# Kernel optimization log

Hardware: AMD Instinct MI355X
Metric: run time of the kernel (lower is better)

Reference implementation:

```python
import jax, jax.numpy as jnp
import numpy as np

PF_DIM = 1024
F_DIM = 1024
LOW = 128
MID = 32  # low_dim // 4
BATCH = 8192


def setup_inputs() -> dict:
    key = jax.random.key(0)
    ks = jax.random.split(key, 10)
    s = lambda fan_in: 1.0 / np.sqrt(fan_in)
    return {
        "f": jax.random.normal(ks[0], (BATCH, F_DIM), jnp.float32),
        "pf": jax.random.normal(ks[1], (BATCH, PF_DIM), jnp.float32),
        # nn.Linear weights are (out, in)
        "proj_f_w": jax.random.uniform(ks[2], (LOW, F_DIM), jnp.float32, -s(F_DIM), s(F_DIM)),
        "proj_f_b": jax.random.uniform(ks[3], (LOW,), jnp.float32, -s(F_DIM), s(F_DIM)),
        "proj_pf_w": jax.random.uniform(ks[4], (LOW, PF_DIM), jnp.float32, -s(PF_DIM), s(PF_DIM)),
        "proj_pf_b": jax.random.uniform(ks[5], (LOW,), jnp.float32, -s(PF_DIM), s(PF_DIM)),
        "proj_f2_w": jax.random.uniform(ks[6], (F_DIM, LOW), jnp.float32, -s(LOW), s(LOW)),
        "proj_f2_b": jax.random.uniform(ks[7], (F_DIM,), jnp.float32, -s(LOW), s(LOW)),
        "pg_w": jax.random.uniform(ks[8], (2 * LOW * MID, LOW), jnp.float32, -s(LOW), s(LOW)),
        "pg_b": jax.random.uniform(ks[9], (2 * LOW * MID,), jnp.float32, -s(LOW), s(LOW)),
    }


def reference(f, pf, proj_f_w, proj_f_b, proj_pf_w, proj_pf_b,
              proj_f2_w, proj_f2_b, pg_w, pg_b):
    b = pf.shape[0]
    # project both inputs to low_dim
    f_low = f @ proj_f_w.T + proj_f_b              # (b, LOW)
    pf_low = pf @ proj_pf_w.T + proj_pf_b          # (b, LOW)
    # per-sample generated weights
    params = pf_low @ pg_w.T + pg_b                # (b, 2*LOW*MID)
    dim = LOW * MID
    p1 = params[:, :dim].reshape(b, LOW, MID)      # (b, LOW, MID)
    p2 = params[:, dim:].reshape(b, MID, LOW)      # (b, MID, LOW)
    # batched tiny MLP: (b,1,LOW)@(b,LOW,MID) -> relu -> @(b,MID,LOW)
    h = jax.nn.relu(jnp.einsum('bl,blm->bm', f_low, p1))
    g = jnp.einsum('bm,bml->bl', h, p2)            # (b, LOW)
    out = g @ proj_f2_w.T + proj_f2_b + f + pf     # (b, F_DIM)
    return out
```

## Files before the change

kernel.cpp:

```cpp
#include <hip/hip_runtime.h>
#include <stdint.h>


typedef __attribute__((ext_vector_type(8))) short bf16x8;
typedef __attribute__((ext_vector_type(4))) float f32x4;

#define MFMA(a, b, c) __builtin_amdgcn_mfma_f32_16x16x32_bf16((a), (b), (c), 0, 0, 0)

__device__ __forceinline__ ushort f2bf(float x) {
    union { float f; uint32_t u; } v; v.f = x;
    return (ushort)((v.u + 0x7FFFu + ((v.u >> 16) & 1u)) >> 16);
}
__device__ __forceinline__ ushort4 f2bf4(float4 v) {
    ushort4 o; o.x = f2bf(v.x); o.y = f2bf(v.y); o.z = f2bf(v.z); o.w = f2bf(v.w); return o;
}
__device__ __forceinline__ float bf2f(ushort u) {
    union { uint32_t i; float f; } v; v.i = ((uint32_t)u) << 16; return v.f;
}

__global__ __launch_bounds__(256) void k0_convert(
    const float* __restrict__ pgw, const float* __restrict__ wf,
    const float* __restrict__ wpf, const float* __restrict__ w2,
    ushort* __restrict__ pg_img, ushort* __restrict__ w_img, ushort* __restrict__ w2_img)
{
    int cid = blockIdx.x * 256 + threadIdx.x;
    const float* src; ushort* dst;
    if (cid < 131072) {
        int lane = cid & 63, ks = (cid >> 6) & 3, T = cid >> 8;
        int j = T * 16 + (lane & 15), k = ks * 32 + (lane >> 4) * 8;
        src = pgw + (size_t)j * 128 + k;
        dst = pg_img + (size_t)cid * 8;
    } else if (cid < 163840) {
        int c = cid - 131072;
        int lane = c & 63, ks = (c >> 6) & 31, lt = (c >> 11) & 7, mat = c >> 14;
        int l = lt * 16 + (lane & 15), k = ks * 32 + (lane >> 4) * 8;
        src = (mat ? wpf : wf) + (size_t)l * 1024 + k;
        dst = w_img + (size_t)c * 8;
    } else {
        int c = cid - 163840;
        int lane = c & 63, ks = (c >> 6) & 3, nt = c >> 8;
        int n = nt * 16 + (lane & 15), k = ks * 32 + (lane >> 4) * 8;
        src = w2 + (size_t)n * 128 + k;
        dst = w2_img + (size_t)c * 8;
    }
    float4 a = ((const float4*)src)[0], b = ((const float4*)src)[1];
    ((ushort4*)dst)[0] = f2bf4(a);
    ((ushort4*)dst)[1] = f2bf4(b);
}

__global__ __launch_bounds__(512, 2) void mega(
    const float* __restrict__ f, const float* __restrict__ pf,
    const ushort* __restrict__ w_img, const float* __restrict__ bfb,
    const float* __restrict__ bpfb, const ushort* __restrict__ pg_img,
    const float* __restrict__ pgb, const ushort* __restrict__ w2_img,
    const float* __restrict__ b2, float* __restrict__ out)
{
    __shared__ __align__(16) char smem[62464];
    ushort* As    = (ushort*)smem;
    ushort* Tr    = (ushort*)smem;
    float*  hred  = (float*)smem;
    float*  hl    = (float*)(smem + 32768);
    float*  gred  = (float*)smem;
    float*  Ls    = (float*)smem;
    ushort* flowT = (ushort*)(smem + 36864);
    ushort* pfrag = (ushort*)(smem + 46080);
    ushort* gfrag = (ushort*)(smem + 54272);

    const int tid = threadIdx.x;
    const int lane = tid & 63, wid = tid >> 6;
    const int q = lane >> 4, r15 = lane & 15;
    const int b0 = blockIdx.x * 32;

    {
        float4 vbuf[8];
#pragma unroll
        for (int rr = 0; rr < 8; rr++) {
            int row = rr * 4 + (tid >> 7);
            vbuf[rr] = *(const float4*)(f + (size_t)(b0 + row) * 1024 + (tid & 127) * 4);
        }
        f32x4 c[2];
        float bias_v = 0.f;
#pragma unroll
        for (int s = 0; s < 4; s++) {
            const int mat = s >> 1, kh = s & 1;
            if (kh == 0) {
                c[0] = (f32x4){0.f, 0.f, 0.f, 0.f};
                c[1] = (f32x4){0.f, 0.f, 0.f, 0.f};
                bias_v = (mat ? bpfb : bfb)[wid * 16 + r15];
            }
            __syncthreads();
#pragma unroll
            for (int rr = 0; rr < 8; rr++) {
                int row = rr * 4 + (tid >> 7);
                *(ushort4*)(As + row * 520 + (tid & 127) * 4) = f2bf4(vbuf[rr]);
            }
            __syncthreads();
            if (s < 3) {
                const int sn = s + 1, matn = sn >> 1, khn = sn & 1;
                const float* srcn = matn ? pf : f;
#pragma unroll
                for (int rr = 0; rr < 8; rr++) {
                    int row = rr * 4 + (tid >> 7);
                    vbuf[rr] = *(const float4*)(srcn + (size_t)(b0 + row) * 1024 + khn * 512 + (tid & 127) * 4);
                }
            }
            const ushort* wb = w_img + (size_t)mat * 131072 + ((size_t)wid * 32 + kh * 16) * 512;
            bf16x8 wfr[4];
#pragma unroll
            for (int p = 0; p < 4; p++) wfr[p] = *(const bf16x8*)(wb + (size_t)p * 512 + lane * 8);
#pragma unroll
            for (int ks = 0; ks < 16; ks++) {
                const int cur = ks & 3;
                bf16x8 a0 = *(const bf16x8*)(As + (size_t)r15 * 520 + ks * 32 + q * 8);
                bf16x8 a1 = *(const bf16x8*)(As + (size_t)(16 + r15) * 520 + ks * 32 + q * 8);
                c[0] = MFMA(a0, wfr[cur], c[0]);
                c[1] = MFMA(a1, wfr[cur], c[1]);
                if (ks + 4 < 16)
                    wfr[cur] = *(const bf16x8*)(wb + (size_t)(ks + 4) * 512 + lane * 8);
            }
            if (s == 1) {
                int l = wid * 16 + r15;
#pragma unroll
                for (int mt = 0; mt < 2; mt++)
#pragma unroll
                    for (int r = 0; r < 4; r++)
                        flowT[l * 36 + mt * 16 + q * 4 + r] = f2bf(c[mt][r] + bias_v);
            }
            if (s == 3) {
                __syncthreads();
                int l = wid * 16 + r15;
#pragma unroll
                for (int mt = 0; mt < 2; mt++)
#pragma unroll
                    for (int r = 0; r < 4; r++)
                        Tr[(mt * 16 + q * 4 + r) * 136 + l] = f2bf(c[mt][r] + bias_v);
                __syncthreads();
                int bt = wid >> 2, ks2 = wid & 3;
                int k0 = ks2 * 32 + (lane >> 4) * 8;
                uint4 tv = *(const uint4*)(Tr + (size_t)(bt * 16 + (lane & 15)) * 136 + k0);
                *(uint4*)(pfrag + (size_t)wid * 512 + lane * 8) = tv;
            }
        }
    }
    __syncthreads();

    bf16x8 bfr[2][4];
#pragma unroll
    for (int ct = 0; ct < 2; ct++)
#pragma unroll
        for (int ks = 0; ks < 4; ks++)
            bfr[ct][ks] = *(const bf16x8*)(pfrag + (size_t)(ct * 4 + ks) * 512 + lane * 8);

    f32x4 hacc[2][2];
    hacc[0][0] = hacc[0][1] = hacc[1][0] = hacc[1][1] = (f32x4){0.f, 0.f, 0.f, 0.f};

    {
        bf16x8 af[4][4];
        f32x4 bvr[4];
#pragma unroll
        for (int t = 0; t < 4; t++) {
            const int tl = wid * 4 + t;
            const ushort* ap = pg_img + (size_t)tl * 2048;
#pragma unroll
            for (int ks = 0; ks < 4; ks++)
                af[t][ks] = *(const bf16x8*)(ap + ks * 512 + lane * 8);
            bvr[t] = *(const f32x4*)(pgb + (size_t)tl * 16 + q * 4);
        }
#pragma unroll
        for (int jg = 0; jg < 8; jg++) {
#pragma unroll
            for (int i = 0; i < 4; i++) {
                const int t = jg * 4 + i, cur = t & 3;
                const int tl = wid * 4 + i;
                const int mh = i & 1;
                const int l_loc = tl >> 1;
                f32x4 bv = bvr[cur];
#pragma unroll
                for (int ct = 0; ct < 2; ct++) {
                    f32x4 cc = (f32x4){0.f, 0.f, 0.f, 0.f};
#pragma unroll
                    for (int ks = 0; ks < 4; ks++) cc = MFMA(af[cur][ks], bfr[ct][ks], cc);
                    float s = bf2f(flowT[(jg * 16 + l_loc) * 36 + ct * 16 + r15]);
#pragma unroll
                    for (int r = 0; r < 4; r++) hacc[mh][ct][r] += s * (cc[r] + bv[r]);
                }
                if (t + 4 < 32) {
                    const int tn = t + 4, jgn = tn >> 2, in = tn & 3;
                    const int tln = jgn * 32 + wid * 4 + in;
                    const ushort* ap = pg_img + (size_t)tln * 2048;
#pragma unroll
                    for (int ks = 0; ks < 4; ks++)
                        af[cur][ks] = *(const bf16x8*)(ap + ks * 512 + lane * 8);
                    bvr[cur] = *(const f32x4*)(pgb + (size_t)tln * 16 + q * 4);
                }
            }
        }
    }
#pragma unroll
    for (int mh = 0; mh < 2; mh++)
#pragma unroll
        for (int ct = 0; ct < 2; ct++)
#pragma unroll
            for (int r = 0; r < 4; r++)
                hred[wid * 1024 + (mh * 16 + q * 4 + r) * 32 + ct * 16 + r15] = hacc[mh][ct][r];
    __syncthreads();
    {
        int m = tid >> 4, bc = (tid & 15) * 2;
        float s0 = 0.f, s1 = 0.f;
#pragma unroll
        for (int w = 0; w < 8; w++) {
            s0 += hred[w * 1024 + m * 32 + bc];
            s1 += hred[w * 1024 + m * 32 + bc + 1];
        }
        hl[m * 32 + bc]     = fmaxf(s0, 0.f);
        hl[m * 32 + bc + 1] = fmaxf(s1, 0.f);
    }
    __syncthreads();

    {
        bf16x8 afc[4][4];
        f32x4 bvc[4];
#pragma unroll
        for (int t = 0; t < 4; t++) {
            const int m = wid + 8 * (t >> 1), lt = t & 1;
            const ushort* ap = pg_img + (size_t)(256 + m * 8 + lt) * 2048;
#pragma unroll
            for (int ks = 0; ks < 4; ks++)
                afc[t][ks] = *(const bf16x8*)(ap + ks * 512 + lane * 8);
            bvc[t] = *(const f32x4*)(pgb + 4096 + (size_t)m * 128 + lt * 16 + q * 4);
        }
#pragma unroll
        for (int lg = 0; lg < 4; lg++) {
            f32x4 gacc[2][2];
            gacc[0][0] = gacc[0][1] = gacc[1][0] = gacc[1][1] = (f32x4){0.f, 0.f, 0.f, 0.f};
#pragma unroll
            for (int ti = 0; ti < 8; ti++) {
                const int t = lg * 8 + ti, cur = t & 3;
                const int m = wid + 8 * (ti >> 1), lt = ti & 1;
                f32x4 bv = bvc[cur];
#pragma unroll
                for (int ct = 0; ct < 2; ct++) {
                    f32x4 cc = (f32x4){0.f, 0.f, 0.f, 0.f};
#pragma unroll
                    for (int ks = 0; ks < 4; ks++) cc = MFMA(afc[cur][ks], bfr[ct][ks], cc);
                    float s = hl[m * 32 + ct * 16 + r15];
#pragma unroll
                    for (int r = 0; r < 4; r++) gacc[lt][ct][r] += s * (cc[r] + bv[r]);
                }
                if (t + 4 < 32) {
                    const int tn = t + 4, lgn = tn >> 3, tin = tn & 7;
                    const int mn = wid + 8 * (tin >> 1), ltn = tin & 1;
                    const ushort* ap = pg_img + (size_t)(256 + mn * 8 + lgn * 2 + ltn) * 2048;
#pragma unroll
                    for (int ks = 0; ks < 4; ks++)
                        afc[cur][ks] = *(const bf16x8*)(ap + ks * 512 + lane * 8);
                    bvc[cur] = *(const f32x4*)(pgb + 4096 + (size_t)mn * 128 + lgn * 32 + ltn * 16 + q * 4);
                }
            }
#pragma unroll
            for (int lt = 0; lt < 2; lt++)
#pragma unroll
                for (int ct = 0; ct < 2; ct++)
#pragma unroll
                    for (int r = 0; r < 4; r++)
                        gred[wid * 1024 + (lt * 16 + q * 4 + r) * 32 + ct * 16 + r15] = gacc[lt][ct][r];
            __syncthreads();
            if (tid < 128) {
                int bt = tid >> 6, ln = tid & 63;
                int b_loc = bt * 16 + (ln & 15);
                int l0 = (ln >> 4) * 8;
                ushort tmp[8];
#pragma unroll
                for (int e = 0; e < 8; e++) {
                    const float* gp = gred + (size_t)(l0 + e) * 32 + b_loc;
                    float s = 0.f;
#pragma unroll
                    for (int w = 0; w < 8; w++) s += gp[w * 1024];
                    tmp[e] = f2bf(s);
                }
                ushort4 lo = {tmp[0], tmp[1], tmp[2], tmp[3]};
                ushort4 hi = {tmp[4], tmp[5], tmp[6], tmp[7]};
                ushort* dst = gfrag + (size_t)(bt * 4 + lg) * 512 + ln * 8;
                ((ushort4*)dst)[0] = lo;
                ((ushort4*)dst)[1] = hi;
            }
            __syncthreads();
        }
    }

    {
        bf16x8 afg[2][4];
#pragma unroll
        for (int mtl = 0; mtl < 2; mtl++)
#pragma unroll
            for (int ks = 0; ks < 4; ks++)
                afg[mtl][ks] = *(const bf16x8*)(gfrag + (size_t)(mtl * 4 + ks) * 512 + lane * 8);

        bf16x8 w2r[2][2][4];
#pragma unroll
        for (int nt = 0; nt < 2; nt++)
#pragma unroll
            for (int ks = 0; ks < 4; ks++)
                w2r[0][nt][ks] = *(const bf16x8*)(w2_img + (size_t)((wid * 2 + nt) * 4 + ks) * 512 + lane * 8);

#pragma unroll
        for (int nb = 0; nb < 4; nb++) {
            const int cur = nb & 1;
            const int n0 = nb * 256;
            float4 fa[4], pa[4];
#pragma unroll
            for (int rr = 0; rr < 4; rr++) {
                const int b = b0 + wid * 4 + rr;
                const size_t gbase = (size_t)b * 1024 + n0 + lane * 4;
                fa[rr] = *(const float4*)(f + gbase);
                pa[rr] = *(const float4*)(pf + gbase);
            }
            float bias_v2[2];
#pragma unroll
            for (int nt = 0; nt < 2; nt++) bias_v2[nt] = b2[nb * 256 + wid * 32 + nt * 16 + r15];
#pragma unroll
            for (int nt = 0; nt < 2; nt++) {
#pragma unroll
                for (int mtl = 0; mtl < 2; mtl++) {
                    f32x4 cc = (f32x4){0.f, 0.f, 0.f, 0.f};
#pragma unroll
                    for (int ks = 0; ks < 4; ks++) cc = MFMA(afg[mtl][ks], w2r[cur][nt][ks], cc);
                    const int nloc = wid * 32 + nt * 16 + r15;
                    const int chunk = nloc >> 5, within = nloc & 31;
#pragma unroll
                    for (int r = 0; r < 4; r++)
                        Ls[(size_t)(mtl * 16 + q * 4 + r) * 288 + chunk * 36 + within] = cc[r] + bias_v2[nt];
                }
            }
            if (nb < 3) {
#pragma unroll
                for (int nt = 0; nt < 2; nt++)
#pragma unroll
                    for (int ks = 0; ks < 4; ks++)
                        w2r[cur ^ 1][nt][ks] = *(const bf16x8*)(w2_img + (size_t)(((nb + 1) * 16 + wid * 2 + nt) * 4 + ks) * 512 + lane * 8);
            }
            __syncthreads();
            {
                const float* ls = Ls + (size_t)(wid * 4) * 288 + (lane >> 3) * 36 + (lane & 7) * 4;
#pragma unroll
                for (int rr = 0; rr < 4; rr++) {
                    const int b = b0 + wid * 4 + rr;
                    const size_t gbase = (size_t)b * 1024 + n0 + lane * 4;
                    float4 lv = *(const float4*)(ls + rr * 288);
                    float4 o;
                    o.x = lv.x + fa[rr].x + pa[rr].x; o.y = lv.y + fa[rr].y + pa[rr].y;
                    o.z = lv.z + fa[rr].z + pa[rr].z; o.w = lv.w + fa[rr].w + pa[rr].w;
                    *(float4*)(out + gbase) = o;
                }
            }
            __syncthreads();
        }
    }
}

extern "C" void kernel_launch(void* const* d_in, const int* in_sizes, int n_in,
                              void* d_out, int out_size, void* d_ws, size_t ws_size,
                              hipStream_t stream)
{
    const float* f    = (const float*)d_in[0];
    const float* pf   = (const float*)d_in[1];
    const float* wf   = (const float*)d_in[2];
    const float* bfb  = (const float*)d_in[3];
    const float* wpf  = (const float*)d_in[4];
    const float* bpfb = (const float*)d_in[5];
    const float* w2   = (const float*)d_in[6];
    const float* b2   = (const float*)d_in[7];
    const float* pgw  = (const float*)d_in[8];
    const float* pgb  = (const float*)d_in[9];

    char* ws = (char*)d_ws;
    ushort* pg_img = (ushort*)(ws + 0);
    ushort* w_img  = (ushort*)(ws + 2097152);
    ushort* w2_img = (ushort*)(ws + 2621440);
    float*  out    = (float*)d_out;

    k0_convert<<<dim3(704), dim3(256), 0, stream>>>(pgw, wf, wpf, w2, pg_img, w_img, w2_img);
    mega<<<dim3(256), dim3(512), 0, stream>>>(f, pf, w_img, bfb, bpfb,
                                              pg_img, pgb, w2_img, b2, out);
}
```

Before: 176.5 us.

## Repartition hypernet weight-gen work across waves to shrink cross-wave reductions

Reassigns the two per-sample weight-generation phases so each wave owns a fixed output slice (mh and l-quarter in phase one, one l-tile in phase two) and accumulates over the contracted index itself. Phase one's cross-wave reduction now sums 4 partials instead of 8. Phase two's per-group LDS reductions and their barriers are removed. Both reduction buffers gain a padded stride of 33 to avoid bank conflicts. W2 register double-buffering is dropped in favour of in-loop loads, which lowers register pressure but exposes load latency.

```diff
diff --git a/kernel.cpp b/kernel.cpp
--- a/kernel.cpp
+++ b/kernel.cpp
@@ -59,8 +59,8 @@
     ushort* As    = (ushort*)smem;
     ushort* Tr    = (ushort*)smem;
     float*  hred  = (float*)smem;
-    float*  hl    = (float*)(smem + 32768);
-    float*  gred  = (float*)smem;
+    float*  hl    = (float*)(smem + 16896);
+    float*  gLDS  = (float*)smem;
     float*  Ls    = (float*)smem;
     ushort* flowT = (ushort*)(smem + 36864);
     ushort* pfrag = (ushort*)(smem + 46080);
@@ -151,66 +151,58 @@
         for (int ks = 0; ks < 4; ks++)
             bfr[ct][ks] = *(const bf16x8*)(pfrag + (size_t)(ct * 4 + ks) * 512 + lane * 8);
 
-    f32x4 hacc[2][2];
-    hacc[0][0] = hacc[0][1] = hacc[1][0] = hacc[1][1] = (f32x4){0.f, 0.f, 0.f, 0.f};
-
-    {
+    {
+        const int mh = wid & 1, lq = wid >> 1;
+        f32x4 hacc[2];
+        hacc[0] = (f32x4){0.f, 0.f, 0.f, 0.f};
+        hacc[1] = (f32x4){0.f, 0.f, 0.f, 0.f};
+
         bf16x8 af[4][4];
-        f32x4 bvr[4];
 #pragma unroll
         for (int t = 0; t < 4; t++) {
-            const int tl = wid * 4 + t;
-            const ushort* ap = pg_img + (size_t)tl * 2048;
+            const int T = (lq * 32 + t) * 2 + mh;
+            const ushort* ap = pg_img + (size_t)T * 2048;
 #pragma unroll
             for (int ks = 0; ks < 4; ks++)
                 af[t][ks] = *(const bf16x8*)(ap + ks * 512 + lane * 8);
-            bvr[t] = *(const f32x4*)(pgb + (size_t)tl * 16 + q * 4);
-        }
-#pragma unroll
-        for (int jg = 0; jg < 8; jg++) {
-#pragma unroll
-            for (int i = 0; i < 4; i++) {
-                const int t = jg * 4 + i, cur = t & 3;
-                const int tl = wid * 4 + i;
-                const int mh = i & 1;
-                const int l_loc = tl >> 1;
-                f32x4 bv = bvr[cur];
-#pragma unroll
-                for (int ct = 0; ct < 2; ct++) {
-                    f32x4 cc = (f32x4){0.f, 0.f, 0.f, 0.f};
-#pragma unroll
-                    for (int ks = 0; ks < 4; ks++) cc = MFMA(af[cur][ks], bfr[ct][ks], cc);
-                    float s = bf2f(flowT[(jg * 16 + l_loc) * 36 + ct * 16 + r15]);
-#pragma unroll
-                    for (int r = 0; r < 4; r++) hacc[mh][ct][r] += s * (cc[r] + bv[r]);
-                }
-                if (t + 4 < 32) {
-                    const int tn = t + 4, jgn = tn >> 2, in = tn & 3;
-                    const int tln = jgn * 32 + wid * 4 + in;
-                    const ushort* ap = pg_img + (size_t)tln * 2048;
-#pragma unroll
-                    for (int ks = 0; ks < 4; ks++)
-                        af[cur][ks] = *(const bf16x8*)(ap + ks * 512 + lane * 8);
-                    bvr[cur] = *(const f32x4*)(pgb + (size_t)tln * 16 + q * 4);
-                }
-            }
-        }
-    }
-#pragma unroll
-    for (int mh = 0; mh < 2; mh++)
+        }
+#pragma unroll
+        for (int t = 0; t < 32; t++) {
+            const int cur = t & 3;
+            const int l = lq * 32 + t;
+            const int T = l * 2 + mh;
+            f32x4 bv = *(const f32x4*)(pgb + (size_t)T * 16 + q * 4);
+#pragma unroll
+            for (int ct = 0; ct < 2; ct++) {
+                f32x4 cc = (f32x4){0.f, 0.f, 0.f, 0.f};
+#pragma unroll
+                for (int ks = 0; ks < 4; ks++) cc = MFMA(af[cur][ks], bfr[ct][ks], cc);
+                float s = bf2f(flowT[l * 36 + ct * 16 + r15]);
+#pragma unroll
+                for (int r = 0; r < 4; r++) hacc[ct][r] += s * (cc[r] + bv[r]);
+            }
+            if (t + 4 < 32) {
+                const int Tn = (l + 4) * 2 + mh;
+                const ushort* ap = pg_img + (size_t)Tn * 2048;
+#pragma unroll
+                for (int ks = 0; ks < 4; ks++)
+                    af[cur][ks] = *(const bf16x8*)(ap + ks * 512 + lane * 8);
+            }
+        }
 #pragma unroll
         for (int ct = 0; ct < 2; ct++)
 #pragma unroll
             for (int r = 0; r < 4; r++)
-                hred[wid * 1024 + (mh * 16 + q * 4 + r) * 32 + ct * 16 + r15] = hacc[mh][ct][r];
+                hred[lq * 1056 + (mh * 16 + q * 4 + r) * 33 + ct * 16 + r15] = hacc[ct][r];
+    }
     __syncthreads();
     {
         int m = tid >> 4, bc = (tid & 15) * 2;
         float s0 = 0.f, s1 = 0.f;
 #pragma unroll
-        for (int w = 0; w < 8; w++) {
-            s0 += hred[w * 1024 + m * 32 + bc];
-            s1 += hred[w * 1024 + m * 32 + bc + 1];
+        for (int w = 0; w < 4; w++) {
+            s0 += hred[w * 1056 + m * 33 + bc];
+            s1 += hred[w * 1056 + m * 33 + bc + 1];
         }
         hl[m * 32 + bc]     = fmaxf(s0, 0.f);
         hl[m * 32 + bc + 1] = fmaxf(s1, 0.f);
@@ -218,75 +210,61 @@
     __syncthreads();
 
     {
+        f32x4 gacc[2];
+        gacc[0] = (f32x4){0.f, 0.f, 0.f, 0.f};
+        gacc[1] = (f32x4){0.f, 0.f, 0.f, 0.f};
+
         bf16x8 afc[4][4];
-        f32x4 bvc[4];
 #pragma unroll
         for (int t = 0; t < 4; t++) {
-            const int m = wid + 8 * (t >> 1), lt = t & 1;
-            const ushort* ap = pg_img + (size_t)(256 + m * 8 + lt) * 2048;
+            const ushort* ap = pg_img + (size_t)(256 + t * 8 + wid) * 2048;
 #pragma unroll
             for (int ks = 0; ks < 4; ks++)
                 afc[t][ks] = *(const bf16x8*)(ap + ks * 512 + lane * 8);
-            bvc[t] = *(const f32x4*)(pgb + 4096 + (size_t)m * 128 + lt * 16 + q * 4);
-        }
-#pragma unroll
-        for (int lg = 0; lg < 4; lg++) {
-            f32x4 gacc[2][2];
-            gacc[0][0] = gacc[0][1] = gacc[1][0] = gacc[1][1] = (f32x4){0.f, 0.f, 0.f, 0.f};
-#pragma unroll
-            for (int ti = 0; ti < 8; ti++) {
-                const int t = lg * 8 + ti, cur = t & 3;
-                const int m = wid + 8 * (ti >> 1), lt = ti & 1;
-                f32x4 bv = bvc[cur];
-#pragma unroll
-                for (int ct = 0; ct < 2; ct++) {
-                    f32x4 cc = (f32x4){0.f, 0.f, 0.f, 0.f};
-#pragma unroll
-                    for (int ks = 0; ks < 4; ks++) cc = MFMA(afc[cur][ks], bfr[ct][ks], cc);
-                    float s = hl[m * 32 + ct * 16 + r15];
-#pragma unroll
-                    for (int r = 0; r < 4; r++) gacc[lt][ct][r] += s * (cc[r] + bv[r]);
-                }
-                if (t + 4 < 32) {
-                    const int tn = t + 4, lgn = tn >> 3, tin = tn & 7;
-                    const int mn = wid + 8 * (tin >> 1), ltn = tin & 1;
-                    const ushort* ap = pg_img + (size_t)(256 + mn * 8 + lgn * 2 + ltn) * 2048;
-#pragma unroll
-                    for (int ks = 0; ks < 4; ks++)
-                        afc[cur][ks] = *(const bf16x8*)(ap + ks * 512 + lane * 8);
-                    bvc[cur] = *(const f32x4*)(pgb + 4096 + (size_t)mn * 128 + lgn * 32 + ltn * 16 + q * 4);
-                }
-            }
-#pragma unroll
-            for (int lt = 0; lt < 2; lt++)
-#pragma unroll
-                for (int ct = 0; ct < 2; ct++)
-#pragma unroll
-                    for (int r = 0; r < 4; r++)
-                        gred[wid * 1024 + (lt * 16 + q * 4 + r) * 32 + ct * 16 + r15] = gacc[lt][ct][r];
-            __syncthreads();
-            if (tid < 128) {
-                int bt = tid >> 6, ln = tid & 63;
-                int b_loc = bt * 16 + (ln & 15);
-                int l0 = (ln >> 4) * 8;
-                ushort tmp[8];
-#pragma unroll
-                for (int e = 0; e < 8; e++) {
-                    const float* gp = gred + (size_t)(l0 + e) * 32 + b_loc;
-                    float s = 0.f;
-#pragma unroll
-                    for (int w = 0; w < 8; w++) s += gp[w * 1024];
-                    tmp[e] = f2bf(s);
-                }
-                ushort4 lo = {tmp[0], tmp[1], tmp[2], tmp[3]};
-                ushort4 hi = {tmp[4], tmp[5], tmp[6], tmp[7]};
-                ushort* dst = gfrag + (size_t)(bt * 4 + lg) * 512 + ln * 8;
-                ((ushort4*)dst)[0] = lo;
-                ((ushort4*)dst)[1] = hi;
-            }
-            __syncthreads();
-        }
-    }
+        }
+#pragma unroll
+        for (int m = 0; m < 32; m++) {
+            const int cur = m & 3;
+            f32x4 bv = *(const f32x4*)(pgb + 4096 + (size_t)m * 128 + wid * 16 + q * 4);
+#pragma unroll
+            for (int ct = 0; ct < 2; ct++) {
+                f32x4 cc = (f32x4){0.f, 0.f, 0.f, 0.f};
+#pragma unroll
+                for (int ks = 0; ks < 4; ks++) cc = MFMA(afc[cur][ks], bfr[ct][ks], cc);
+                float s = hl[m * 32 + ct * 16 + r15];
+#pragma unroll
+                for (int r = 0; r < 4; r++) gacc[ct][r] += s * (cc[r] + bv[r]);
+            }
+            if (m + 4 < 32) {
+                const int mn = m + 4;
+                const ushort* ap = pg_img + (size_t)(256 + mn * 8 + wid) * 2048;
+#pragma unroll
+                for (int ks = 0; ks < 4; ks++)
+                    afc[cur][ks] = *(const bf16x8*)(ap + ks * 512 + lane * 8);
+            }
+        }
+#pragma unroll
+        for (int ct = 0; ct < 2; ct++)
+#pragma unroll
+            for (int r = 0; r < 4; r++)
+                gLDS[(size_t)(wid * 16 + q * 4 + r) * 33 + ct * 16 + r15] = gacc[ct][r];
+    }
+    __syncthreads();
+    {
+        const int bt = wid >> 2, ksl = wid & 3;
+        const int bloc = bt * 16 + (lane & 15);
+        const int l0 = ksl * 32 + (lane >> 4) * 8;
+        ushort tmp[8];
+#pragma unroll
+        for (int e = 0; e < 8; e++)
+            tmp[e] = f2bf(gLDS[(size_t)(l0 + e) * 33 + bloc]);
+        ushort4 lo = {tmp[0], tmp[1], tmp[2], tmp[3]};
+        ushort4 hi = {tmp[4], tmp[5], tmp[6], tmp[7]};
+        ushort* dst = gfrag + (size_t)wid * 512 + lane * 8;
+        ((ushort4*)dst)[0] = lo;
+        ((ushort4*)dst)[1] = hi;
+    }
+    __syncthreads();
 
     {
         bf16x8 afg[2][4];
@@ -296,16 +274,8 @@
             for (int ks = 0; ks < 4; ks++)
                 afg[mtl][ks] = *(const bf16x8*)(gfrag + (size_t)(mtl * 4 + ks) * 512 + lane * 8);
 
-        bf16x8 w2r[2][2][4];
-#pragma unroll
-        for (int nt = 0; nt < 2; nt++)
-#pragma unroll
-            for (int ks = 0; ks < 4; ks++)
-                w2r[0][nt][ks] = *(const bf16x8*)(w2_img + (size_t)((wid * 2 + nt) * 4 + ks) * 512 + lane * 8);
-
 #pragma unroll
         for (int nb = 0; nb < 4; nb++) {
-            const int cur = nb & 1;
             const int n0 = nb * 256;
             float4 fa[4], pa[4];
 #pragma unroll
@@ -318,26 +288,25 @@
             float bias_v2[2];
 #pragma unroll
             for (int nt = 0; nt < 2; nt++) bias_v2[nt] = b2[nb * 256 + wid * 32 + nt * 16 + r15];
+            bf16x8 w2r[2][4];
+#pragma unroll
+            for (int nt = 0; nt < 2; nt++)
+#pragma unroll
+                for (int ks = 0; ks < 4; ks++)
+                    w2r[nt][ks] = *(const bf16x8*)(w2_img + (size_t)((nb * 16 + wid * 2 + nt) * 4 + ks) * 512 + lane * 8);
 #pragma unroll
             for (int nt = 0; nt < 2; nt++) {
 #pragma unroll
                 for (int mtl = 0; mtl < 2; mtl++) {
                     f32x4 cc = (f32x4){0.f, 0.f, 0.f, 0.f};
 #pragma unroll
-                    for (int ks = 0; ks < 4; ks++) cc = MFMA(afg[mtl][ks], w2r[cur][nt][ks], cc);
+                    for (int ks = 0; ks < 4; ks++) cc = MFMA(afg[mtl][ks], w2r[nt][ks], cc);
                     const int nloc = wid * 32 + nt * 16 + r15;
                     const int chunk = nloc >> 5, within = nloc & 31;
 #pragma unroll
                     for (int r = 0; r < 4; r++)
                         Ls[(size_t)(mtl * 16 + q * 4 + r) * 288 + chunk * 36 + within] = cc[r] + bias_v2[nt];
                 }
-            }
-            if (nb < 3) {
-#pragma unroll
-                for (int nt = 0; nt < 2; nt++)
-#pragma unroll
-                    for (int ks = 0; ks < 4; ks++)
-                        w2r[cur ^ 1][nt][ks] = *(const bf16x8*)(w2_img + (size_t)(((nb + 1) * 16 + wid * 2 + nt) * 4 + ks) * 512 + lane * 8);
             }
             __syncthreads();
             {
```

After: 241.7 us. 1.37x slower.
